# Performance work log

Measured on AMD Instinct MI355X. Metric: run time of the kernel, lower is better.

## Reference

```python
import jax, jax.numpy as jnp
import numpy as np
from jax import lax

V, E, H = 32000, 256, 512
B, S_SRC, S_TGT = 32, 128, 64


def setup_inputs() -> dict:
    key = jax.random.key(0)
    ks = jax.random.split(key, 16)
    n = lambda k, shp: jax.random.normal(k, shp, dtype=jnp.float32) * 0.05
    return {
        "src": jax.random.randint(ks[0], (B, S_SRC), 0, V, dtype=jnp.int32),
        "tgt": jax.random.randint(ks[1], (B, S_TGT), 0, V, dtype=jnp.int32),
        "enc_emb": n(ks[2], (V, E)),
        "enc_Wih": n(ks[3], (4 * H, E)),
        "enc_Whh": n(ks[4], (4 * H, H)),
        "enc_b": n(ks[5], (4 * H,)),
        "attn_W": n(ks[6], (H, 2 * H)),
        "attn_b": n(ks[7], (H,)),
        "attn_v": jax.random.uniform(ks[8], (H,), dtype=jnp.float32),
        "dec_emb": n(ks[9], (V, E)),
        "dec_Wih": n(ks[10], (4 * H, E + H)),
        "dec_Whh": n(ks[11], (4 * H, H)),
        "dec_b": n(ks[12], (4 * H,)),
        "out_W": n(ks[13], (V, H)),
        "out_b": n(ks[14], (V,)),
    }


def _lstm_cell(x, h, c, Wih, Whh, b):
    # PyTorch gate order: i, f, g, o. b = b_ih + b_hh fused.
    z = x @ Wih.T + h @ Whh.T + b  # [B, 4H]
    i, f, g, o = jnp.split(z, 4, axis=-1)
    c_new = jax.nn.sigmoid(f) * c + jax.nn.sigmoid(i) * jnp.tanh(g)
    h_new = jax.nn.sigmoid(o) * jnp.tanh(c_new)
    return h_new, c_new


def reference(src, tgt, enc_emb, enc_Wih, enc_Whh, enc_b, attn_W, attn_b,
              attn_v, dec_emb, dec_Wih, dec_Whh, dec_b, out_W, out_b):
    b = src.shape[0]
    h0 = jnp.zeros((b, H), dtype=enc_emb.dtype)
    c0 = jnp.zeros((b, H), dtype=enc_emb.dtype)

    # ---- Encoder: single-layer LSTM over src ----
    emb_src = enc_emb[src]  # [B, S_src, E]

    def enc_step(carry, x_t):
        h, c = carry
        h, c = _lstm_cell(x_t, h, c, enc_Wih, enc_Whh, enc_b)
        return (h, c), h

    (h, c), enc_out = lax.scan(enc_step, (h0, c0), emb_src.transpose(1, 0, 2))
    enc_out = enc_out.transpose(1, 0, 2)  # [B, S_src, H]

    # attn_W acts on cat([hidden, enc]); split into hidden and encoder parts.
    W_h = attn_W[:, :H]   # [H, H]
    W_e = attn_W[:, H:]   # [H, H]
    enc_proj = jnp.einsum('bsh,kh->bsk', enc_out, W_e)  # precomputed [B, S, H]

    # ---- Decoder with per-step Bahdanau attention ----
    emb_tgt = dec_emb[tgt].transpose(1, 0, 2)  # [T, B, E]

    def dec_step(carry, e_t):
        h, c = carry
        energy = jnp.tanh(enc_proj + (h @ W_h.T + attn_b)[:, None, :])  # [B,S,H]
        score = energy @ attn_v                                          # [B,S]
        a = jax.nn.softmax(score, axis=1)
        context = jnp.einsum('bs,bsh->bh', a, enc_out)                   # [B,H]
        x = jnp.concatenate([e_t, context], axis=-1)                     # [B,E+H]
        h, c = _lstm_cell(x, h, c, dec_Wih, dec_Whh, dec_b)
        return (h, c), h

    _, dec_h = lax.scan(dec_step, (h, c), emb_tgt)
    dec_h = dec_h.transpose(1, 0, 2)  # [B, T, H]

    return dec_h @ out_W.T + out_b  # [B, T, V]
```

## Files before the change

kernel.cpp:

```cpp
#include <hip/hip_runtime.h>

#define B_    32
#define SSRC  128
#define STGT  64
#define E_    256
#define H_    512
#define G4    2048
#define V_    32000

typedef unsigned short u16;
typedef short bf16x8 __attribute__((ext_vector_type(8)));
typedef float f32x4 __attribute__((ext_vector_type(4)));

__device__ __forceinline__ u16 f2b(float f) {
  unsigned u = __float_as_uint(f);
  u += 0x7FFFu + ((u >> 16) & 1u);
  return (u16)(u >> 16);
}
__device__ __forceinline__ float b2f(u16 h) {
  return __uint_as_float(((unsigned)h) << 16);
}
__device__ __forceinline__ unsigned pk2(float lo, float hi) {
  return (unsigned)f2b(lo) | (((unsigned)f2b(hi)) << 16);
}
__device__ __forceinline__ float sigm(float x) { return 1.0f / (1.0f + __expf(-x)); }
__device__ __forceinline__ float tanh_(float x) { return 1.0f - 2.0f / (1.0f + __expf(2.0f * x)); }

#if defined(__has_builtin)
#if __has_builtin(__builtin_amdgcn_fdot2_f32_bf16)
#define HAS_DOT2 1
#endif
#endif
#ifdef HAS_DOT2
typedef __bf16 b162 __attribute__((ext_vector_type(2)));
__device__ __forceinline__ float dot2u(unsigned a, unsigned b, float acc) {
  return __builtin_amdgcn_fdot2_f32_bf16(__builtin_bit_cast(b162, a),
                                         __builtin_bit_cast(b162, b), acc, false);
}
#else
__device__ __forceinline__ float dot2u(unsigned a, unsigned b, float acc) {
  acc += __uint_as_float(a << 16) * __uint_as_float(b << 16);
  acc += __uint_as_float(a & 0xffff0000u) * __uint_as_float(b & 0xffff0000u);
  return acc;
}
#endif
__device__ __forceinline__ float dot4(uint4 w, uint4 h, float acc) {
  return dot2u(w.w, h.w, dot2u(w.z, h.z, dot2u(w.y, h.y, dot2u(w.x, h.x, acc))));
}

__device__ __forceinline__ int swz64(int c) {
  return (c & ~3) | ((c & 3) ^ ((c >> 3) & 3));
}

__device__ __forceinline__ uint4 cload4(const void* p) {
  uint4 r;
  asm volatile("global_load_dwordx4 %0, %1, off sc0 sc1\n\ts_waitcnt vmcnt(0)"
               : "=&v"(r) : "v"(p) : "memory");
  return r;
}
__device__ __forceinline__ void cload4x2(uint4& a, uint4& b, const void* pa, const void* pb) {
  asm volatile("global_load_dwordx4 %0, %2, off sc0 sc1\n\t"
               "global_load_dwordx4 %1, %3, off sc0 sc1\n\t"
               "s_waitcnt vmcnt(0)"
               : "=&v"(a), "=&v"(b) : "v"(pa), "v"(pb) : "memory");
}
__device__ __forceinline__ void cstoreu(unsigned* p, unsigned v) {
  asm volatile("global_store_dword %0, %1, off sc0 sc1" :: "v"(p), "v"(v) : "memory");
}
__device__ __forceinline__ void cstore4(unsigned* p, uint4 v) {
  cstoreu(p + 0, v.x);
  cstoreu(p + 1, v.y);
  cstoreu(p + 2, v.z);
  cstoreu(p + 3, v.w);
}

__device__ __forceinline__ void gbar(int* flags, int myid, int target) {
  asm volatile("s_waitcnt vmcnt(0)" ::: "memory");
  __syncthreads();
  if (threadIdx.x == 0)
    __hip_atomic_store(flags + myid, target, __ATOMIC_RELAXED, __HIP_MEMORY_SCOPE_AGENT);
  if (threadIdx.x < 64) {
    int l = threadIdx.x & 31;
    while (__hip_atomic_load(flags + l, __ATOMIC_RELAXED, __HIP_MEMORY_SCOPE_AGENT) < target)
      __builtin_amdgcn_s_sleep(1);
  }
  __syncthreads();
  asm volatile("" ::: "memory");
}

__global__ void prep_kernel(const int* __restrict__ src, const int* __restrict__ tgt,
                            const float* __restrict__ enc_emb, const float* __restrict__ dec_emb,
                            const float* __restrict__ enc_Wih, const float* __restrict__ dec_Wih,
                            const float* __restrict__ attn_W, const float* __restrict__ out_W,
                            u16* __restrict__ A_enc, u16* __restrict__ A_dec,
                            u16* __restrict__ WihE, u16* __restrict__ WihD,
                            u16* __restrict__ Web, u16* __restrict__ WihCp,
                            u16* __restrict__ outWb)
{
  const long n_outw = (long)V_ * H_;
  const long n_aenc = (long)B_ * SSRC * E_;
  const long n_adec = (long)B_ * STGT * E_;
  const long n_wih  = (long)G4 * E_;
  const long n_web  = (long)H_ * H_;
  const long n_wcp  = (long)G4 * H_;
  const long total = n_outw + n_aenc + n_adec + 2 * n_wih + n_web + n_wcp;
  for (long i = (long)blockIdx.x * blockDim.x + threadIdx.x; i < total;
       i += (long)gridDim.x * blockDim.x) {
    long x = i;
    if (x < n_outw) { outWb[x] = f2b(out_W[x]); continue; }
    x -= n_outw;
    if (x < n_aenc) {
      int row = (int)(x >> 8), e = (int)(x & 255);
      A_enc[x] = f2b(enc_emb[(size_t)src[row] * E_ + e]);
      continue;
    }
    x -= n_aenc;
    if (x < n_adec) {
      int row = (int)(x >> 8), e = (int)(x & 255);
      A_dec[x] = f2b(dec_emb[(size_t)tgt[row] * E_ + e]);
      continue;
    }
    x -= n_adec;
    if (x < n_wih) { WihE[x] = f2b(enc_Wih[x]); continue; }
    x -= n_wih;
    if (x < n_wih) {
      int r = (int)(x >> 8), e = (int)(x & 255);
      WihD[x] = f2b(dec_Wih[(size_t)r * 768 + e]);
      continue;
    }
    x -= n_wih;
    if (x < n_web) {
      int d = (int)(x >> 9), k = (int)(x & 511);
      Web[x] = f2b(attn_W[(size_t)d * 1024 + 512 + k]);
      continue;
    }
    x -= n_web;
    {
      int n = (int)(x >> 9), k = (int)(x & 511);
      int gb = n >> 6, gate = (n >> 4) & 3, jl = n & 15;
      int orig = gate * 512 + gb * 16 + jl;
      WihCp[x] = f2b(dec_Wih[(size_t)orig * 768 + 256 + k]);
    }
  }
}

template<int KTOT, bool OBF>
__global__ __launch_bounds__(256, 2) void gemm_nt(
    const u16* __restrict__ A, const u16* __restrict__ Bm,
    const float* __restrict__ bias, void* __restrict__ Cv, int M, int N)
{
  int nbm = M >> 7;
  int bn = blockIdx.x / nbm;
  int bm = blockIdx.x % nbm;
  int w = threadIdx.x >> 6, l = threadIdx.x & 63;
  int wr = w >> 1, wc = w & 1;
  int m0 = bm * 128 + wr * 64, n0 = bn * 128 + wc * 64;
  int lr = l & 15, ko = (l >> 4) * 8;
  f32x4 acc[4][4] = {};
  const u16* Ap = A + (size_t)(m0 + lr) * KTOT + ko;
  const u16* Bp = Bm + (size_t)(n0 + lr) * KTOT + ko;
  for (int k0 = 0; k0 < KTOT; k0 += 32) {
    bf16x8 af[4], bfr[4];
#pragma unroll
    for (int i = 0; i < 4; ++i) af[i] = *(const bf16x8*)(Ap + (size_t)i * 16 * KTOT + k0);
#pragma unroll
    for (int i = 0; i < 4; ++i) bfr[i] = *(const bf16x8*)(Bp + (size_t)i * 16 * KTOT + k0);
#pragma unroll
    for (int i = 0; i < 4; ++i)
#pragma unroll
      for (int j = 0; j < 4; ++j)
        acc[i][j] = __builtin_amdgcn_mfma_f32_16x16x32_bf16(af[i], bfr[j], acc[i][j], 0, 0, 0);
  }
  int rbase = (l >> 4) * 4;
#pragma unroll
  for (int i = 0; i < 4; ++i) {
#pragma unroll
    for (int j = 0; j < 4; ++j) {
      int gn = n0 + j * 16 + lr;
      float bv = bias ? bias[gn] : 0.f;
#pragma unroll
      for (int r = 0; r < 4; ++r) {
        int gm = m0 + i * 16 + rbase + r;
        float v = acc[i][j][r] + bv;
        if (OBF) ((u16*)Cv)[(size_t)gm * N + gn] = f2b(v);
        else     ((float*)Cv)[(size_t)gm * N + gn] = v;
      }
    }
  }
}

__device__ __forceinline__ void zgemv64(int tid, const uint4* Wu, const uint4* Hu,
                                        float (*part)[64][4]) {
  int rq = tid >> 4, kq = tid & 15;
  float acc[4][4] = {};
#pragma unroll
  for (int u = 0; u < 4; ++u) {
    int sc = swz64(kq * 4 + u);
    uint4 h0 = Hu[sc], h1 = Hu[64 + sc], h2 = Hu[128 + sc], h3 = Hu[192 + sc];
#pragma unroll
    for (int r = 0; r < 4; ++r) {
      uint4 wv = Wu[(rq * 4 + r) * 64 + sc];
      acc[r][0] = dot4(wv, h0, acc[r][0]);
      acc[r][1] = dot4(wv, h1, acc[r][1]);
      acc[r][2] = dot4(wv, h2, acc[r][2]);
      acc[r][3] = dot4(wv, h3, acc[r][3]);
    }
  }
#pragma unroll
  for (int r = 0; r < 4; ++r) {
    float4 v = {acc[r][0], acc[r][1], acc[r][2], acc[r][3]};
    *(float4*)&part[kq][(rq * 4 + r) ^ (kq & 7)][0] = v;
  }
}

template<typename GrowF>
__device__ __forceinline__ void fillw64(int tid, const float* Wsrc, uint4* Wu, GrowF grow) {
#pragma unroll 4
  for (int i = 0; i < 16; ++i) {
    int idx4 = tid + i * 256;
    int row = idx4 >> 6, c = idx4 & 63;
    const float* s = Wsrc + (size_t)grow(row) * 512 + c * 8;
    float4 a = *(const float4*)s, b4 = *(const float4*)(s + 4);
    uint4 pkv = {pk2(a.x, a.y), pk2(a.z, a.w), pk2(b4.x, b4.y), pk2(b4.z, b4.w)};
    Wu[row * 64 + swz64(c)] = pkv;
  }
}

__global__ __launch_bounds__(256, 1) void encoder_kernel(
    const float* __restrict__ enc_Whh, const u16* __restrict__ encXW,
    unsigned* __restrict__ h16buf ,
    float* __restrict__ cfin, u16* __restrict__ eo_g, int* __restrict__ bars)
{
  const int tid = threadIdx.x;
  const int g = blockIdx.x & 7;
  const int gb = blockIdx.x >> 3;
  const int b0 = g * 4;
  const int ds0 = gb * 16;
  int* flags = bars + g * 64;
  int ep_ = 0;

  __shared__ uint4 encW4[64 * 64];
  __shared__ uint4 hl16[4 * 64];
  __shared__ float part[16][64][4];
  __shared__ float zx[4][64];
  __shared__ float cS[4][16];

  if (tid < 64) cS[tid >> 4][tid & 15] = 0.f;
  fillw64(tid, enc_Whh, encW4, [&](int row) { return (row >> 4) * 512 + ds0 + (row & 15); });
  __syncthreads();

  for (int t = 0; t < SSRC; ++t) {
    {
      int row = tid >> 6, c = tid & 63;
      uint4 v = cload4((const uint4*)h16buf + (size_t)(t & 1) * 2048 + (b0 + row) * 64 + c);
      hl16[row * 64 + swz64(c)] = v;
    }
    __syncthreads();
    zgemv64(tid, encW4, hl16, part);
    __syncthreads();
    {
      int b_l = tid >> 6, rl = tid & 63;
      float z = 0.f;
#pragma unroll
      for (int kq = 0; kq < 16; ++kq) z += part[kq][rl ^ (kq & 7)][b_l];
      int grow = (rl >> 4) * 512 + ds0 + (rl & 15);
      z += b2f(encXW[((size_t)(b0 + b_l) * SSRC + t) * G4 + grow]);
      zx[b_l][rl] = z;
    }
    __syncthreads();
    if (tid < 64) {
      int bl = tid >> 4, jl = tid & 15;
      float iv = zx[bl][jl], fv = zx[bl][16 + jl], gv = zx[bl][32 + jl], ov = zx[bl][48 + jl];
      float cn = sigm(fv) * cS[bl][jl] + sigm(iv) * tanh_(gv);
      float hn = sigm(ov) * tanh_(cn);
      cS[bl][jl] = cn;
      eo_g[((size_t)(b0 + bl) * SSRC + t) * H_ + ds0 + jl] = f2b(hn);
      float hn1 = __shfl_down(hn, 1);
      if ((jl & 1) == 0)
        cstoreu(h16buf + (size_t)((t + 1) & 1) * 8192 + (size_t)(b0 + bl) * 256 + gb * 8 + (jl >> 1),
                pk2(hn, hn1));
    }
    gbar(flags, gb, ++ep_);
  }
  if (tid < 64)
    cfin[(size_t)(b0 + (tid >> 4)) * H_ + ds0 + (tid & 15)] = cS[tid >> 4][tid & 15];
}

__global__ __launch_bounds__(256, 1) void decoder_kernel(
    const float* __restrict__ dec_Whh, const float* __restrict__ attn_W,
    const float* __restrict__ attn_b, const float* __restrict__ attn_v,
    const u16* __restrict__ eprojb, const u16* __restrict__ decXW,
    const u16* __restrict__ eoPb,
    unsigned* __restrict__ hd16 , const float* __restrict__ cfin,
    float* __restrict__ qg , float* __restrict__ scoreb ,
    u16* __restrict__ dech, int* __restrict__ bars)
{
  const int tid = threadIdx.x;
  const int g = blockIdx.x & 7;
  const int gb = blockIdx.x >> 3;
  const int b0 = g * 4;
  const int ds0 = gb * 16;
  int* flags = bars + g * 64;
  int ep_ = 0;

  __shared__ uint4 decW4[64 * 64];
  __shared__ uint4 Whb4[16 * 64];
  __shared__ uint4 hl16[4 * 64];
  __shared__ float part[16][64][4];
  __shared__ float partE[8][64][4];
  __shared__ float4 qf4[4 * 128];
  __shared__ float4 vf4[128];
  __shared__ float scoreS[4][128];
  __shared__ float aS[4][128];
  __shared__ float zx[4][64];
  __shared__ __align__(16) float qS[4][16];
  __shared__ __align__(16) float scr16[4][4];
  __shared__ float cS[4][16];
  __shared__ float bS[16];

  if (tid < 64) cS[tid >> 4][tid & 15] = cfin[(size_t)(b0 + (tid >> 4)) * H_ + ds0 + (tid & 15)];
  if (tid < 16) bS[tid] = attn_b[ds0 + tid];
  if (tid < 128) {
    float4 v = *(const float4*)(attn_v + tid * 4);
    vf4[tid ^ ((tid >> 3) & 7)] = v;
  }
  fillw64(tid, dec_Whh, decW4, [&](int row) { return (row >> 4) * 512 + ds0 + (row & 15); });
#pragma unroll
  for (int i = 0; i < 4; ++i) {
    int idx4 = tid + i * 256;
    int row = idx4 >> 6, c = idx4 & 63;
    const float* s = attn_W + (size_t)(ds0 + row) * 1024 + c * 8;
    float4 a = *(const float4*)s, b4 = *(const float4*)(s + 4);
    uint4 pkv = {pk2(a.x, a.y), pk2(a.z, a.w), pk2(b4.x, b4.y), pk2(b4.z, b4.w)};
    Whb4[row * 64 + (c ^ (row & 7))] = pkv;
  }
  __syncthreads();

  for (int t = 0; t < STGT; ++t) {
    {
      int row = tid >> 6, c = tid & 63;
      uint4 v = cload4((const uint4*)hd16 + (b0 + row) * 64 + c);
      hl16[row * 64 + swz64(c)] = v;
    }
    __syncthreads();
    {
      int b_l = tid >> 6, d_l = (tid >> 2) & 15, kq4 = tid & 3;
      float acc = 0.f;
#pragma unroll
      for (int u = 0; u < 16; ++u) {
        int c = kq4 * 16 + u;
        uint4 wv = Whb4[d_l * 64 + (c ^ (d_l & 7))];
        uint4 hv = hl16[b_l * 64 + swz64(c)];
        acc = dot4(wv, hv, acc);
      }
      acc += __shfl_xor(acc, 1);
      acc += __shfl_xor(acc, 2);
      if (kq4 == 0) qS[b_l][d_l] = acc + bS[d_l];
    }
    __syncthreads();
    if (tid < 16) {
      float4 v = *(float4*)&qS[tid >> 2][(tid & 3) * 4];
      cstore4((unsigned*)(qg + (size_t)(g * 4 + (tid >> 2)) * 512 + ds0 + (tid & 3) * 4),
              *(uint4*)&v);
    }
    gbar(flags, gb, ++ep_);

    {
      int b_l = tid >> 6, c = tid & 63;
      uint4 a, b4;
      const float* sp = qg + (size_t)(g * 4 + b_l) * 512 + c * 8;
      cload4x2(a, b4, sp, sp + 4);
      int lw0 = c * 2, lw1 = c * 2 + 1;
      qf4[b_l * 128 + (lw0 ^ ((lw0 >> 3) & 7))] = *(float4*)&a;
      qf4[b_l * 128 + (lw1 ^ ((lw1 >> 3) & 7))] = *(float4*)&b4;
    }
    __syncthreads();
    {
      int p = tid >> 4, lane16 = tid & 15;
      int b_l = p >> 2, s_l = p & 3;
      int s = gb * 4 + s_l;
      const uint4* ep = (const uint4*)(eprojb + ((size_t)(b0 + b_l) * SSRC + s) * H_) + lane16 * 4;
      uint4 e0 = ep[0], e1 = ep[1], e2 = ep[2], e3 = ep[3];
      unsigned ev[8] = {e0.x, e0.y, e0.z, e0.w, e1.x, e1.y, e1.z, e1.w};
      unsigned ev2[8] = {e2.x, e2.y, e2.z, e2.w, e3.x, e3.y, e3.z, e3.w};
      float acc = 0.f;
#pragma unroll
      for (int i = 0; i < 8; ++i) {
        int lr = lane16 * 8 + i;
        float4 q = qf4[b_l * 128 + (lr ^ ((lr >> 3) & 7))];
        float4 vv = vf4[lr ^ ((lr >> 3) & 7)];
        unsigned lo = (i < 4) ? ev[i * 2] : ev2[(i - 4) * 2];
        unsigned hi = (i < 4) ? ev[i * 2 + 1] : ev2[(i - 4) * 2 + 1];
        acc += vv.x * tanh_(b2f((u16)(lo & 0xffff)) + q.x);
        acc += vv.y * tanh_(b2f((u16)(lo >> 16)) + q.y);
        acc += vv.z * tanh_(b2f((u16)(hi & 0xffff)) + q.z);
        acc += vv.w * tanh_(b2f((u16)(hi >> 16)) + q.w);
      }
      acc += __shfl_xor(acc, 1);
      acc += __shfl_xor(acc, 2);
      acc += __shfl_xor(acc, 4);
      acc += __shfl_xor(acc, 8);
      if (lane16 == 0) scr16[b_l][s_l] = acc;
    }
    __syncthreads();
    if (tid < 4) {
      float4 v = *(float4*)&scr16[tid][0];
      cstore4((unsigned*)(scoreb + (size_t)(g * 4 + tid) * 128 + gb * 4), *(uint4*)&v);
    }
    gbar(flags, gb, ++ep_);

    if (tid < 128) {
      int row = tid >> 5, c4 = tid & 31;
      uint4 vv = cload4(scoreb + (size_t)(g * 4 + row) * 128 + c4 * 4);
      *(float4*)&scoreS[row][c4 * 4] = *(float4*)&vv;
    }
    zgemv64(tid, decW4, hl16, part);
    __syncthreads();
    {
      int w = tid >> 6, lane = tid & 63;
      float s1 = scoreS[w][lane], s2v = scoreS[w][64 + lane];
      float m = fmaxf(s1, s2v);
#pragma unroll
      for (int off = 32; off; off >>= 1) m = fmaxf(m, __shfl_xor(m, off));
      float e1 = __expf(s1 - m), e2 = __expf(s2v - m);
      float sm = e1 + e2;
#pragma unroll
      for (int off = 32; off; off >>= 1) sm += __shfl_xor(sm, off);
      float inv = 1.0f / sm;
      aS[w][lane] = e1 * inv;
      aS[w][64 + lane] = e2 * inv;
    }
    __syncthreads();
    {
      int sq = tid >> 5, cp = tid & 31;
      const unsigned* eoPu = (const unsigned*)eoPb;
      float a0 = 0.f, a1 = 0.f, a2 = 0.f, a3 = 0.f, a4 = 0.f, a5 = 0.f, a6 = 0.f, a7 = 0.f;
#pragma unroll 4
      for (int s = sq * 16; s < sq * 16 + 16; ++s) {
        unsigned u0 = eoPu[((size_t)(b0 + 0) * SSRC + s) * 1024 + gb * 32 + cp];
        unsigned u1 = eoPu[((size_t)(b0 + 1) * SSRC + s) * 1024 + gb * 32 + cp];
        unsigned u2 = eoPu[((size_t)(b0 + 2) * SSRC + s) * 1024 + gb * 32 + cp];
        unsigned u3 = eoPu[((size_t)(b0 + 3) * SSRC + s) * 1024 + gb * 32 + cp];
        float w0 = aS[0][s], w1 = aS[1][s], w2 = aS[2][s], w3 = aS[3][s];
        a0 += w0 * b2f((u16)(u0 & 0xffff)); a1 += w0 * b2f((u16)(u0 >> 16));
        a2 += w1 * b2f((u16)(u1 & 0xffff)); a3 += w1 * b2f((u16)(u1 >> 16));
        a4 += w2 * b2f((u16)(u2 & 0xffff)); a5 += w2 * b2f((u16)(u2 >> 16));
        a6 += w3 * b2f((u16)(u3 & 0xffff)); a7 += w3 * b2f((u16)(u3 >> 16));
      }
      float4 lo = {a0, a2, a4, a6}, hi = {a1, a3, a5, a7};
      *(float4*)&partE[sq][cp * 2][0] = lo;
      *(float4*)&partE[sq][cp * 2 + 1][0] = hi;
    }
    __syncthreads();
    {
      int b_l = tid >> 6, rl = tid & 63;
      float z = 0.f;
#pragma unroll
      for (int kq = 0; kq < 16; ++kq) z += part[kq][rl ^ (kq & 7)][b_l];
#pragma unroll
      for (int sq = 0; sq < 8; ++sq) z += partE[sq][rl][b_l];
      int grow = (rl >> 4) * 512 + ds0 + (rl & 15);
      z += b2f(decXW[((size_t)(b0 + b_l) * STGT + t) * G4 + grow]);
      zx[b_l][rl] = z;
    }
    __syncthreads();
    if (tid < 64) {
      int bl = tid >> 4, jl = tid & 15;
      float iv = zx[bl][jl], fv = zx[bl][16 + jl], gv = zx[bl][32 + jl], ov = zx[bl][48 + jl];
      float cn = sigm(fv) * cS[bl][jl] + sigm(iv) * tanh_(gv);
      float hn = sigm(ov) * tanh_(cn);
      cS[bl][jl] = cn;
      dech[((size_t)(b0 + bl) * STGT + t) * H_ + ds0 + jl] = f2b(hn);
      float hn1 = __shfl_down(hn, 1);
      if ((jl & 1) == 0)
        cstoreu(hd16 + (size_t)(b0 + bl) * 256 + gb * 8 + (jl >> 1), pk2(hn, hn1));
    }
    gbar(flags, gb, ++ep_);
  }
}

#define OFF_BARE   0u
#define OFF_BARD   2048u
#define OFF_H16    4096u
#define OFF_CFIN   69632u
#define OFF_QG     135168u
#define OFF_SCORE  200704u
#define OFF_AENC   262144u
#define OFF_ADEC   2359296u
#define OFF_WIHE   3407872u
#define OFF_WIHD   4456448u
#define OFF_WEB    5505024u
#define OFF_WIHCP  6029312u
#define OFF_OUTW   8126464u
#define OFF_ENCXW  40894464u
#define OFF_DECXW  57671680u
#define OFF_EO     66060288u
#define OFF_EPROJ  70254592u
#define OFF_DECH   74448896u

extern "C" void kernel_launch(void* const* d_in, const int* in_sizes, int n_in,
                              void* d_out, int out_size, void* d_ws, size_t ws_size,
                              hipStream_t stream)
{
  const int*   src     = (const int*)d_in[0];
  const int*   tgt     = (const int*)d_in[1];
  const float* enc_emb = (const float*)d_in[2];
  const float* enc_Wih = (const float*)d_in[3];
  const float* enc_Whh = (const float*)d_in[4];
  const float* enc_b   = (const float*)d_in[5];
  const float* attn_W  = (const float*)d_in[6];
  const float* attn_b  = (const float*)d_in[7];
  const float* attn_v  = (const float*)d_in[8];
  const float* dec_emb = (const float*)d_in[9];
  const float* dec_Wih = (const float*)d_in[10];
  const float* dec_Whh = (const float*)d_in[11];
  const float* dec_b   = (const float*)d_in[12];
  const float* out_W   = (const float*)d_in[13];
  const float* out_b   = (const float*)d_in[14];

  char* ws = (char*)d_ws;
  int*      barE   = (int*)(ws + OFF_BARE);
  int*      barD   = (int*)(ws + OFF_BARD);
  unsigned* h16buf = (unsigned*)(ws + OFF_H16);
  float*    cfin   = (float*)(ws + OFF_CFIN);
  float*    qg     = (float*)(ws + OFF_QG);
  float*    scoreb = (float*)(ws + OFF_SCORE);
  u16*      A_enc  = (u16*)(ws + OFF_AENC);
  u16*      A_dec  = (u16*)(ws + OFF_ADEC);
  u16*      WihE   = (u16*)(ws + OFF_WIHE);
  u16*      WihD   = (u16*)(ws + OFF_WIHD);
  u16*      Web    = (u16*)(ws + OFF_WEB);
  u16*      WihCp  = (u16*)(ws + OFF_WIHCP);
  u16*      outWb  = (u16*)(ws + OFF_OUTW);
  u16*      encXW  = (u16*)(ws + OFF_ENCXW);
  u16*      eoPb   = (u16*)(ws + OFF_ENCXW);
  u16*      decXW  = (u16*)(ws + OFF_DECXW);
  u16*      eo_g   = (u16*)(ws + OFF_EO);
  u16*      eprojb = (u16*)(ws + OFF_EPROJ);
  u16*      dech   = (u16*)(ws + OFF_DECH);

  (void)hipMemsetAsync(d_ws, 0, OFF_H16 + 65536, stream);

  prep_kernel<<<2048, 256, 0, stream>>>(src, tgt, enc_emb, dec_emb, enc_Wih, dec_Wih,
                                        attn_W, out_W, A_enc, A_dec, WihE, WihD, Web, WihCp, outWb);

  gemm_nt<256, true><<<512, 256, 0, stream>>>(A_enc, WihE, enc_b, (void*)encXW, 4096, 2048);
  gemm_nt<256, true><<<256, 256, 0, stream>>>(A_dec, WihD, dec_b, (void*)decXW, 2048, 2048);

  encoder_kernel<<<256, 256, 0, stream>>>(enc_Whh, encXW, h16buf, cfin, eo_g, barE);

  gemm_nt<512, true><<<128, 256, 0, stream>>>(eo_g, Web, nullptr, (void*)eprojb, 4096, 512);
  gemm_nt<512, true><<<512, 256, 0, stream>>>(eo_g, WihCp, nullptr, (void*)eoPb, 4096, 2048);

  decoder_kernel<<<256, 256, 0, stream>>>(dec_Whh, attn_W, attn_b, attn_v,
                                          eprojb, decXW, eoPb, h16buf, cfin,
                                          qg, scoreb, dech, barD);

  gemm_nt<512, false><<<4000, 256, 0, stream>>>(dech, outWb, out_b, d_out, 2048, 32000);
}
```

Measured before the change: 1.555 ms.

## Replace grid flag barriers with tagged 64-bit data words in recurrent kernels

Removes the per-step global flag barriers in the encoder and decoder LSTM loops. Each exchanged value (hidden state, attention query, partial scores) is now stored as a 64-bit word holding the payload and a step tag, and consumers poll until the tag matches. Blocks therefore synchronise point-to-point on exactly the data they need instead of waiting on all blocks in the group. The decoder's recurrent gemv is also moved ahead of the query exchange so it can overlap the wait. The cost is doubled exchange-buffer traffic and more atomic loads while spinning.

After: 1.655 ms. 6.4% more time.

```diff
diff --git a/kernel.cpp b/kernel.cpp
--- a/kernel.cpp
+++ b/kernel.cpp
@@ -9,6 +9,7 @@
 #define V_    32000
 
 typedef unsigned short u16;
+typedef unsigned long long u64b;
 typedef short bf16x8 __attribute__((ext_vector_type(8)));
 typedef float f32x4 __attribute__((ext_vector_type(4)));
 
@@ -52,40 +53,33 @@
   return (c & ~3) | ((c & 3) ^ ((c >> 3) & 3));
 }
 
-__device__ __forceinline__ uint4 cload4(const void* p) {
-  uint4 r;
-  asm volatile("global_load_dwordx4 %0, %1, off sc0 sc1\n\ts_waitcnt vmcnt(0)"
-               : "=&v"(r) : "v"(p) : "memory");
-  return r;
-}
-__device__ __forceinline__ void cload4x2(uint4& a, uint4& b, const void* pa, const void* pb) {
-  asm volatile("global_load_dwordx4 %0, %2, off sc0 sc1\n\t"
-               "global_load_dwordx4 %1, %3, off sc0 sc1\n\t"
-               "s_waitcnt vmcnt(0)"
-               : "=&v"(a), "=&v"(b) : "v"(pa), "v"(pb) : "memory");
-}
-__device__ __forceinline__ void cstoreu(unsigned* p, unsigned v) {
-  asm volatile("global_store_dword %0, %1, off sc0 sc1" :: "v"(p), "v"(v) : "memory");
-}
-__device__ __forceinline__ void cstore4(unsigned* p, uint4 v) {
-  cstoreu(p + 0, v.x);
-  cstoreu(p + 1, v.y);
-  cstoreu(p + 2, v.z);
-  cstoreu(p + 3, v.w);
-}
-
-__device__ __forceinline__ void gbar(int* flags, int myid, int target) {
-  asm volatile("s_waitcnt vmcnt(0)" ::: "memory");
-  __syncthreads();
-  if (threadIdx.x == 0)
-    __hip_atomic_store(flags + myid, target, __ATOMIC_RELAXED, __HIP_MEMORY_SCOPE_AGENT);
-  if (threadIdx.x < 64) {
-    int l = threadIdx.x & 31;
-    while (__hip_atomic_load(flags + l, __ATOMIC_RELAXED, __HIP_MEMORY_SCOPE_AGENT) < target)
-      __builtin_amdgcn_s_sleep(1);
-  }
-  __syncthreads();
-  asm volatile("" ::: "memory");
+__device__ __forceinline__ void tstore(u64b* p, unsigned payload, unsigned tag) {
+  __hip_atomic_store(p, ((u64b)tag << 32) | payload, __ATOMIC_RELAXED, __HIP_MEMORY_SCOPE_AGENT);
+}
+__device__ __forceinline__ u64b tload(const u64b* p) {
+  return __hip_atomic_load(p, __ATOMIC_RELAXED, __HIP_MEMORY_SCOPE_AGENT);
+}
+__device__ __forceinline__ void poll4(const u64b* p, unsigned tag,
+                                      u64b& a, u64b& b, u64b& c, u64b& d) {
+  for (;;) {
+    a = tload(p + 0); b = tload(p + 1); c = tload(p + 2); d = tload(p + 3);
+    if ((((unsigned)(a >> 32)) == tag) & (((unsigned)(b >> 32)) == tag) &
+        (((unsigned)(c >> 32)) == tag) & (((unsigned)(d >> 32)) == tag)) return;
+    __builtin_amdgcn_s_sleep(1);
+  }
+}
+__device__ __forceinline__ void poll8(const u64b* p, unsigned tag,
+                                      u64b& a, u64b& b, u64b& c, u64b& d,
+                                      u64b& e, u64b& f, u64b& g_, u64b& h) {
+  for (;;) {
+    a = tload(p + 0); b = tload(p + 1); c = tload(p + 2); d = tload(p + 3);
+    e = tload(p + 4); f = tload(p + 5); g_ = tload(p + 6); h = tload(p + 7);
+    if ((((unsigned)(a >> 32)) == tag) & (((unsigned)(b >> 32)) == tag) &
+        (((unsigned)(c >> 32)) == tag) & (((unsigned)(d >> 32)) == tag) &
+        (((unsigned)(e >> 32)) == tag) & (((unsigned)(f >> 32)) == tag) &
+        (((unsigned)(g_ >> 32)) == tag) & (((unsigned)(h >> 32)) == tag)) return;
+    __builtin_amdgcn_s_sleep(1);
+  }
 }
 
 __global__ void prep_kernel(const int* __restrict__ src, const int* __restrict__ tgt,
@@ -228,16 +222,14 @@
 
 __global__ __launch_bounds__(256, 1) void encoder_kernel(
     const float* __restrict__ enc_Whh, const u16* __restrict__ encXW,
-    unsigned* __restrict__ h16buf ,
-    float* __restrict__ cfin, u16* __restrict__ eo_g, int* __restrict__ bars)
+    u64b* __restrict__ hbufE , u64b* __restrict__ hd64 ,
+    float* __restrict__ cfin, u16* __restrict__ eo_g)
 {
   const int tid = threadIdx.x;
   const int g = blockIdx.x & 7;
   const int gb = blockIdx.x >> 3;
   const int b0 = g * 4;
   const int ds0 = gb * 16;
-  int* flags = bars + g * 64;
-  int ep_ = 0;
 
   __shared__ uint4 encW4[64 * 64];
   __shared__ uint4 hl16[4 * 64];
@@ -252,8 +244,11 @@
   for (int t = 0; t < SSRC; ++t) {
     {
       int row = tid >> 6, c = tid & 63;
-      uint4 v = cload4((const uint4*)h16buf + (size_t)(t & 1) * 2048 + (b0 + row) * 64 + c);
-      hl16[row * 64 + swz64(c)] = v;
+      const u64b* p = hbufE + (size_t)(t & 1) * 8192 + (size_t)(b0 + row) * 256 + c * 4;
+      u64b v0, v1, v2, v3;
+      poll4(p, (unsigned)t, v0, v1, v2, v3);
+      uint4 hv = {(unsigned)v0, (unsigned)v1, (unsigned)v2, (unsigned)v3};
+      hl16[row * 64 + swz64(c)] = hv;
     }
     __syncthreads();
     zgemv64(tid, encW4, hl16, part);
@@ -276,11 +271,14 @@
       cS[bl][jl] = cn;
       eo_g[((size_t)(b0 + bl) * SSRC + t) * H_ + ds0 + jl] = f2b(hn);
       float hn1 = __shfl_down(hn, 1);
-      if ((jl & 1) == 0)
-        cstoreu(h16buf + (size_t)((t + 1) & 1) * 8192 + (size_t)(b0 + bl) * 256 + gb * 8 + (jl >> 1),
-                pk2(hn, hn1));
-    }
-    gbar(flags, gb, ++ep_);
+      if ((jl & 1) == 0) {
+        unsigned pk = pk2(hn, hn1);
+        size_t w = (size_t)(b0 + bl) * 256 + gb * 8 + (jl >> 1);
+        tstore(hbufE + (size_t)((t + 1) & 1) * 8192 + w, pk, (unsigned)(t + 1));
+        if (t == SSRC - 1) tstore(hd64 + w, pk, 1u);
+      }
+    }
+    __syncthreads();
   }
   if (tid < 64)
     cfin[(size_t)(b0 + (tid >> 4)) * H_ + ds0 + (tid & 15)] = cS[tid >> 4][tid & 15];
@@ -291,17 +289,15 @@
     const float* __restrict__ attn_b, const float* __restrict__ attn_v,
     const u16* __restrict__ eprojb, const u16* __restrict__ decXW,
     const u16* __restrict__ eoPb,
-    unsigned* __restrict__ hd16 , const float* __restrict__ cfin,
-    float* __restrict__ qg , float* __restrict__ scoreb ,
-    u16* __restrict__ dech, int* __restrict__ bars)
+    u64b* __restrict__ hd64, const float* __restrict__ cfin,
+    u64b* __restrict__ qg64 , u64b* __restrict__ scoreb64 ,
+    u16* __restrict__ dech)
 {
   const int tid = threadIdx.x;
   const int g = blockIdx.x & 7;
   const int gb = blockIdx.x >> 3;
   const int b0 = g * 4;
   const int ds0 = gb * 16;
-  int* flags = bars + g * 64;
-  int ep_ = 0;
 
   __shared__ uint4 decW4[64 * 64];
   __shared__ uint4 Whb4[16 * 64];
@@ -339,8 +335,11 @@
   for (int t = 0; t < STGT; ++t) {
     {
       int row = tid >> 6, c = tid & 63;
-      uint4 v = cload4((const uint4*)hd16 + (b0 + row) * 64 + c);
-      hl16[row * 64 + swz64(c)] = v;
+      const u64b* p = hd64 + (size_t)(b0 + row) * 256 + c * 4;
+      u64b v0, v1, v2, v3;
+      poll4(p, (unsigned)(t + 1), v0, v1, v2, v3);
+      uint4 hv = {(unsigned)v0, (unsigned)v1, (unsigned)v2, (unsigned)v3};
+      hl16[row * 64 + swz64(c)] = hv;
     }
     __syncthreads();
     {
@@ -349,9 +348,7 @@
 #pragma unroll
       for (int u = 0; u < 16; ++u) {
         int c = kq4 * 16 + u;
-        uint4 wv = Whb4[d_l * 64 + (c ^ (d_l & 7))];
-        uint4 hv = hl16[b_l * 64 + swz64(c)];
-        acc = dot4(wv, hv, acc);
+        acc = dot4(Whb4[d_l * 64 + (c ^ (d_l & 7))], hl16[b_l * 64 + swz64(c)], acc);
       }
       acc += __shfl_xor(acc, 1);
       acc += __shfl_xor(acc, 2);
@@ -359,20 +356,27 @@
     }
     __syncthreads();
     if (tid < 16) {
-      float4 v = *(float4*)&qS[tid >> 2][(tid & 3) * 4];
-      cstore4((unsigned*)(qg + (size_t)(g * 4 + (tid >> 2)) * 512 + ds0 + (tid & 3) * 4),
-              *(uint4*)&v);
-    }
-    gbar(flags, gb, ++ep_);
+      int bl = tid >> 2, i0 = (tid & 3) * 4;
+      u64b* qp = qg64 + (size_t)(g * 4 + bl) * 512 + ds0 + i0;
+#pragma unroll
+      for (int k = 0; k < 4; ++k)
+        tstore(qp + k, __float_as_uint(qS[bl][i0 + k]), (unsigned)(t + 1));
+    }
+    zgemv64(tid, decW4, hl16, part);
+    __syncthreads();
 
     {
       int b_l = tid >> 6, c = tid & 63;
-      uint4 a, b4;
-      const float* sp = qg + (size_t)(g * 4 + b_l) * 512 + c * 8;
-      cload4x2(a, b4, sp, sp + 4);
+      const u64b* p = qg64 + (size_t)(g * 4 + b_l) * 512 + c * 8;
+      u64b v0, v1, v2, v3, v4, v5, v6, v7;
+      poll8(p, (unsigned)(t + 1), v0, v1, v2, v3, v4, v5, v6, v7);
       int lw0 = c * 2, lw1 = c * 2 + 1;
-      qf4[b_l * 128 + (lw0 ^ ((lw0 >> 3) & 7))] = *(float4*)&a;
-      qf4[b_l * 128 + (lw1 ^ ((lw1 >> 3) & 7))] = *(float4*)&b4;
+      float4 q0 = {__uint_as_float((unsigned)v0), __uint_as_float((unsigned)v1),
+                   __uint_as_float((unsigned)v2), __uint_as_float((unsigned)v3)};
+      float4 q1 = {__uint_as_float((unsigned)v4), __uint_as_float((unsigned)v5),
+                   __uint_as_float((unsigned)v6), __uint_as_float((unsigned)v7)};
+      qf4[b_l * 128 + (lw0 ^ ((lw0 >> 3) & 7))] = q0;
+      qf4[b_l * 128 + (lw1 ^ ((lw1 >> 3) & 7))] = q1;
     }
     __syncthreads();
     {
@@ -404,17 +408,22 @@
     }
     __syncthreads();
     if (tid < 4) {
-      float4 v = *(float4*)&scr16[tid][0];
-      cstore4((unsigned*)(scoreb + (size_t)(g * 4 + tid) * 128 + gb * 4), *(uint4*)&v);
-    }
-    gbar(flags, gb, ++ep_);
+      u64b* sp = scoreb64 + (size_t)(g * 4 + tid) * 128 + gb * 4;
+#pragma unroll
+      for (int k = 0; k < 4; ++k)
+        tstore(sp + k, __float_as_uint(scr16[tid][k]), (unsigned)(t + 1));
+    }
 
     if (tid < 128) {
       int row = tid >> 5, c4 = tid & 31;
-      uint4 vv = cload4(scoreb + (size_t)(g * 4 + row) * 128 + c4 * 4);
-      *(float4*)&scoreS[row][c4 * 4] = *(float4*)&vv;
-    }
-    zgemv64(tid, decW4, hl16, part);
+      const u64b* p = scoreb64 + (size_t)(g * 4 + row) * 128 + c4 * 4;
+      u64b v0, v1, v2, v3;
+      poll4(p, (unsigned)(t + 1), v0, v1, v2, v3);
+      scoreS[row][c4 * 4 + 0] = __uint_as_float((unsigned)v0);
+      scoreS[row][c4 * 4 + 1] = __uint_as_float((unsigned)v1);
+      scoreS[row][c4 * 4 + 2] = __uint_as_float((unsigned)v2);
+      scoreS[row][c4 * 4 + 3] = __uint_as_float((unsigned)v3);
+    }
     __syncthreads();
     {
       int w = tid >> 6, lane = tid & 63;
@@ -458,7 +467,7 @@
 #pragma unroll
       for (int kq = 0; kq < 16; ++kq) z += part[kq][rl ^ (kq & 7)][b_l];
 #pragma unroll
-      for (int sq = 0; sq < 8; ++sq) z += partE[sq][rl][b_l];
+      for (int sq2 = 0; sq2 < 8; ++sq2) z += partE[sq2][rl][b_l];
       int grow = (rl >> 4) * 512 + ds0 + (rl & 15);
       z += b2f(decXW[((size_t)(b0 + b_l) * STGT + t) * G4 + grow]);
       zx[b_l][rl] = z;
@@ -473,30 +482,30 @@
       dech[((size_t)(b0 + bl) * STGT + t) * H_ + ds0 + jl] = f2b(hn);
       float hn1 = __shfl_down(hn, 1);
       if ((jl & 1) == 0)
-        cstoreu(hd16 + (size_t)(b0 + bl) * 256 + gb * 8 + (jl >> 1), pk2(hn, hn1));
-    }
-    gbar(flags, gb, ++ep_);
-  }
-}
-
-#define OFF_BARE   0u
-#define OFF_BARD   2048u
-#define OFF_H16    4096u
-#define OFF_CFIN   69632u
-#define OFF_QG     135168u
-#define OFF_SCORE  200704u
-#define OFF_AENC   262144u
-#define OFF_ADEC   2359296u
-#define OFF_WIHE   3407872u
-#define OFF_WIHD   4456448u
-#define OFF_WEB    5505024u
-#define OFF_WIHCP  6029312u
-#define OFF_OUTW   8126464u
-#define OFF_ENCXW  40894464u
-#define OFF_DECXW  57671680u
-#define OFF_EO     66060288u
-#define OFF_EPROJ  70254592u
-#define OFF_DECH   74448896u
+        tstore(hd64 + (size_t)(b0 + bl) * 256 + gb * 8 + (jl >> 1), pk2(hn, hn1),
+               (unsigned)(t + 2));
+    }
+    __syncthreads();
+  }
+}
+
+#define OFF_HBE    0u
+#define OFF_HD     131072u
+#define OFF_QG     196608u
+#define OFF_SC     327680u
+#define OFF_CFIN   360448u
+#define OFF_AENC   524288u
+#define OFF_ADEC   2621440u
+#define OFF_WIHE   3670016u
+#define OFF_WIHD   4718592u
+#define OFF_WEB    5767168u
+#define OFF_WIHCP  6291456u
+#define OFF_OUTW   8388608u
+#define OFF_ENCXW  41943040u
+#define OFF_DECXW  58720256u
+#define OFF_EPROJ  67108864u
+#define OFF_EO     71303168u
+#define OFF_DECH   75497472u
 
 extern "C" void kernel_launch(void* const* d_in, const int* in_sizes, int n_in,
                               void* d_out, int out_size, void* d_ws, size_t ws_size,
@@ -519,27 +528,26 @@
   const float* out_b   = (const float*)d_in[14];
 
   char* ws = (char*)d_ws;
-  int*      barE   = (int*)(ws + OFF_BARE);
-  int*      barD   = (int*)(ws + OFF_BARD);
-  unsigned* h16buf = (unsigned*)(ws + OFF_H16);
-  float*    cfin   = (float*)(ws + OFF_CFIN);
-  float*    qg     = (float*)(ws + OFF_QG);
-  float*    scoreb = (float*)(ws + OFF_SCORE);
-  u16*      A_enc  = (u16*)(ws + OFF_AENC);
-  u16*      A_dec  = (u16*)(ws + OFF_ADEC);
-  u16*      WihE   = (u16*)(ws + OFF_WIHE);
-  u16*      WihD   = (u16*)(ws + OFF_WIHD);
-  u16*      Web    = (u16*)(ws + OFF_WEB);
-  u16*      WihCp  = (u16*)(ws + OFF_WIHCP);
-  u16*      outWb  = (u16*)(ws + OFF_OUTW);
-  u16*      encXW  = (u16*)(ws + OFF_ENCXW);
-  u16*      eoPb   = (u16*)(ws + OFF_ENCXW);
-  u16*      decXW  = (u16*)(ws + OFF_DECXW);
-  u16*      eo_g   = (u16*)(ws + OFF_EO);
-  u16*      eprojb = (u16*)(ws + OFF_EPROJ);
-  u16*      dech   = (u16*)(ws + OFF_DECH);
-
-  (void)hipMemsetAsync(d_ws, 0, OFF_H16 + 65536, stream);
+  u64b*  hbufE  = (u64b*)(ws + OFF_HBE);
+  u64b*  hd64   = (u64b*)(ws + OFF_HD);
+  u64b*  qg64   = (u64b*)(ws + OFF_QG);
+  u64b*  scb64  = (u64b*)(ws + OFF_SC);
+  float* cfin   = (float*)(ws + OFF_CFIN);
+  u16*   A_enc  = (u16*)(ws + OFF_AENC);
+  u16*   A_dec  = (u16*)(ws + OFF_ADEC);
+  u16*   WihE   = (u16*)(ws + OFF_WIHE);
+  u16*   WihD   = (u16*)(ws + OFF_WIHD);
+  u16*   Web    = (u16*)(ws + OFF_WEB);
+  u16*   WihCp  = (u16*)(ws + OFF_WIHCP);
+  u16*   outWb  = (u16*)(ws + OFF_OUTW);
+  u16*   encXW  = (u16*)(ws + OFF_ENCXW);
+  u16*   eoPb   = (u16*)(ws + OFF_ENCXW);
+  u16*   decXW  = (u16*)(ws + OFF_DECXW);
+  u16*   eprojb = (u16*)(ws + OFF_EPROJ);
+  u16*   eo_g   = (u16*)(ws + OFF_EO);
+  u16*   dech   = (u16*)(ws + OFF_DECH);
+
+  (void)hipMemsetAsync(d_ws, 0, 360448, stream);
 
   prep_kernel<<<2048, 256, 0, stream>>>(src, tgt, enc_emb, dec_emb, enc_Wih, dec_Wih,
                                         attn_W, out_W, A_enc, A_dec, WihE, WihD, Web, WihCp, outWb);
@@ -547,14 +555,14 @@
   gemm_nt<256, true><<<512, 256, 0, stream>>>(A_enc, WihE, enc_b, (void*)encXW, 4096, 2048);
   gemm_nt<256, true><<<256, 256, 0, stream>>>(A_dec, WihD, dec_b, (void*)decXW, 2048, 2048);
 
-  encoder_kernel<<<256, 256, 0, stream>>>(enc_Whh, encXW, h16buf, cfin, eo_g, barE);
+  encoder_kernel<<<256, 256, 0, stream>>>(enc_Whh, encXW, hbufE, hd64, cfin, eo_g);
 
   gemm_nt<512, true><<<128, 256, 0, stream>>>(eo_g, Web, nullptr, (void*)eprojb, 4096, 512);
   gemm_nt<512, true><<<512, 256, 0, stream>>>(eo_g, WihCp, nullptr, (void*)eoPb, 4096, 2048);
 
   decoder_kernel<<<256, 256, 0, stream>>>(dec_Whh, attn_W, attn_b, attn_v,
-                                          eprojb, decXW, eoPb, h16buf, cfin,
-                                          qg, scoreb, dech, barD);
+                                          eprojb, decXW, eoPb, hd64, cfin,
+                                          qg64, scb64, dech);
 
   gemm_nt<512, false><<<4000, 256, 0, stream>>>(dech, outWb, out_b, d_out, 2048, 32000);
 }
```
